# Performance work log

Measured on AMD Instinct MI355X. Metric: run time of the kernel, lower is better.

## Reference

```python
import jax, jax.numpy as jnp
import numpy as np

K = 3           # kernel_size
PAD = (K - 1) // 2
GC = 16         # group_channels (hardcoded in module)
EPS = 1e-5      # BatchNorm eps


def _extract_patches(x):
    # x: [B,C,H,W] -> [B,C,K*K,H,W], patch index = kh*K+kw (torch Unfold order)
    B, C, H, W = x.shape
    xp = jnp.pad(x, ((0, 0), (0, 0), (PAD, PAD), (PAD, PAD)))
    slices = [xp[:, :, i:i + H, j:j + W] for i in range(K) for j in range(K)]
    return jnp.stack(slices, axis=2)


def setup_inputs() -> dict:
    key = jax.random.key(0)
    ks = jax.random.split(key, 6)
    B, C, H, W = 4, 256, 128, 128
    Cr = C // 4                 # reduction_ratio = 4
    G = C // GC                 # groups = 16
    x = jax.random.normal(ks[0], (B, C, H, W), dtype=jnp.float32)
    # conv1: 1x1, C -> C/4, bias-free (followed by BN) + ReLU
    w1 = jax.random.normal(ks[1], (Cr, C), dtype=jnp.float32) * (1.0 / np.sqrt(C))
    bn_gamma = jnp.ones((Cr,), jnp.float32)
    bn_beta = jnp.zeros((Cr,), jnp.float32)
    bn_mean = jax.random.normal(ks[2], (Cr,), dtype=jnp.float32) * 0.1
    bn_var = jax.random.uniform(ks[3], (Cr,), dtype=jnp.float32, minval=0.5, maxval=1.5)
    # conv2: 1x1, C/4 -> K*K*groups, with bias, no norm/act
    w2 = jax.random.normal(ks[4], (K * K * G, Cr), dtype=jnp.float32) * (1.0 / np.sqrt(Cr))
    b2 = jax.random.normal(ks[5], (K * K * G,), dtype=jnp.float32) * 0.01
    return {"x": x, "w1": w1, "bn_gamma": bn_gamma, "bn_beta": bn_beta,
            "bn_mean": bn_mean, "bn_var": bn_var, "w2": w2, "b2": b2}


def reference(x, w1, bn_gamma, bn_beta, bn_mean, bn_var, w2, b2):
    B, C, H, W = x.shape
    G = C // GC
    # conv1 (1x1) + BN (inference) + ReLU
    h1 = jnp.einsum('bchw,oc->bohw', x, w1)
    inv_std = jax.lax.rsqrt(bn_var + EPS)
    h1 = (h1 - bn_mean[None, :, None, None]) * (bn_gamma * inv_std)[None, :, None, None] \
         + bn_beta[None, :, None, None]
    h1 = jax.nn.relu(h1)
    # conv2 (1x1) -> per-pixel dynamic kernels [B, G, K*K, H, W]
    wk = jnp.einsum('bchw,oc->bohw', h1, w2) + b2[None, :, None, None]
    wk = wk.reshape(B, G, K * K, H, W)
    # unfold x -> [B, G, GC, K*K, H, W], multiply by kernels and reduce over K*K
    patches = _extract_patches(x).reshape(B, G, GC, K * K, H, W)
    out = jnp.einsum('bgkhw,bgckhw->bgchw', wk, patches)
    return out.reshape(B, C, H, W)
```

## Files before the change

### kernel.cpp

```cpp
#include <hip/hip_runtime.h>

#define B_   4
#define C_   256
#define CR_  64
#define H_   128
#define W_   128
#define HW_  (H_ * W_)
#define G_   16
#define GC_  16
#define KO_  144
#define EPS_ 1e-5f

typedef __bf16 bf16x8 __attribute__((ext_vector_type(8)));
typedef __bf16 bf16x4 __attribute__((ext_vector_type(4)));
typedef float  f32x4  __attribute__((ext_vector_type(4)));

#define SX2 132
#define WKS 132

__global__ void prep_kernel(const float* __restrict__ w1,
                            const float* __restrict__ gamma,
                            const float* __restrict__ beta,
                            const float* __restrict__ mean,
                            const float* __restrict__ var,
                            const float* __restrict__ w2,
                            __bf16* __restrict__ w1frag,
                            __bf16* __restrict__ w2frag,
                            float* __restrict__ bias2) {
    int idx = blockIdx.x * 256 + threadIdx.x;
    if (idx < 16384) {
        int kc = idx >> 11, r = idx & 2047;
        int mt = r >> 9, l = (r >> 3) & 63, j = r & 7;
        int o = mt * 16 + (l & 15);
        int c = kc * 32 + 8 * (l >> 4) + j;
        float alpha = gamma[o] * rsqrtf(var[o] + EPS_);
        w1frag[idx] = (__bf16)(w1[o * C_ + c] * alpha);
        if (idx < CR_) {
            float a2 = gamma[idx] * rsqrtf(var[idx] + EPS_);
            bias2[idx] = beta[idx] - mean[idx] * a2;
        }
    } else if (idx < 16384 + 9216) {
        int i2 = idx - 16384;
        int mt = i2 >> 10, r = i2 & 1023;
        int kc2 = r >> 9, l = (r >> 3) & 63, j = r & 7;
        int o2 = mt * 16 + (l & 15);
        int cc = kc2 * 32 + 8 * (l >> 4) + j;
        w2frag[i2] = (__bf16)(w2[o2 * CR_ + cc]);
    }
}

__global__ __launch_bounds__(512, 4) void fused_kernel(
        const float* __restrict__ x,
        const __bf16* __restrict__ w1frag,
        const float* __restrict__ bias2,
        const __bf16* __restrict__ w2frag,
        const float* __restrict__ b2,
        float* __restrict__ out) {
    __shared__ __align__(16) char smem[71808];
    __bf16* xs    = (__bf16*)smem;
    __bf16* hbuf  = (__bf16*)(smem + 16896);
    __bf16* wkbuf = (__bf16*)(smem + 33792);
    __bf16* cbuf  = (__bf16*)smem;

    const int tid  = threadIdx.x;
    const int lane = tid & 63;
    const int wave = tid >> 6;
    const int wm = wave >> 2, wn = wave & 3;
    const int g = lane >> 4, n = lane & 15;

    const int bid = (blockIdx.x & 7) * 64 + (blockIdx.x >> 3);
    const int b   = bid >> 7;
    const int h   = bid & 127;

    const float* xrow = x + (size_t)b * C_ * HW_ + h * W_;

#pragma unroll
    for (int i = 0; i < 2; ++i) {
        int s = tid + 512 * i;
        int cl = s >> 5, f4i = s & 31;
        float4 v = *(const float4*)&xrow[(size_t)cl * HW_ + f4i * 4];
        *(bf16x4*)&xs[cl * SX2 + f4i * 4] =
            bf16x4{(__bf16)v.x, (__bf16)v.y, (__bf16)v.z, (__bf16)v.w};
    }
    __syncthreads();

    f32x4 acc1[2][2];
#pragma unroll
    for (int m = 0; m < 2; ++m)
#pragma unroll
        for (int t = 0; t < 2; ++t) acc1[m][t] = f32x4{0.f, 0.f, 0.f, 0.f};

    for (int kc = 0; kc < 8; ++kc) {
        const int buf = kc & 1;
        float4 nf[2];
        if (kc < 7) {
#pragma unroll
            for (int i = 0; i < 2; ++i) {
                int s = tid + 512 * i;
                int cl = s >> 5, f4i = s & 31;
                nf[i] = *(const float4*)&xrow[(size_t)(32 * (kc + 1) + cl) * HW_ + f4i * 4];
            }
        }
        bf16x8 a0 = *(const bf16x8*)&w1frag[((kc * 4 + 2 * wm + 0) * 64 + lane) * 8];
        bf16x8 a1 = *(const bf16x8*)&w1frag[((kc * 4 + 2 * wm + 1) * 64 + lane) * 8];
        const int base = buf * (32 * SX2);
        bf16x8 bt[2];
#pragma unroll
        for (int t = 0; t < 2; ++t)
#pragma unroll
            for (int j = 0; j < 8; ++j)
                bt[t][j] = xs[base + (8 * g + j) * SX2 + (2 * wn + t) * 16 + n];
#pragma unroll
        for (int t = 0; t < 2; ++t) {
            acc1[0][t] = __builtin_amdgcn_mfma_f32_16x16x32_bf16(a0, bt[t], acc1[0][t], 0, 0, 0);
            acc1[1][t] = __builtin_amdgcn_mfma_f32_16x16x32_bf16(a1, bt[t], acc1[1][t], 0, 0, 0);
        }
        if (kc < 7) {
            const int nb = (buf ^ 1) * (32 * SX2);
#pragma unroll
            for (int i = 0; i < 2; ++i) {
                int s = tid + 512 * i;
                int cl = s >> 5, f4i = s & 31;
                *(bf16x4*)&xs[nb + cl * SX2 + f4i * 4] =
                    bf16x4{(__bf16)nf[i].x, (__bf16)nf[i].y, (__bf16)nf[i].z, (__bf16)nf[i].w};
            }
        }
        __syncthreads();
    }

#pragma unroll
    for (int m = 0; m < 2; ++m) {
        const int Mo = (2 * wm + m) * 16 + 4 * g;
        float4 bv = *(const float4*)&bias2[Mo];
        float bj[4] = {bv.x, bv.y, bv.z, bv.w};
#pragma unroll
        for (int t = 0; t < 2; ++t) {
            const int px = (2 * wn + t) * 16 + n;
#pragma unroll
            for (int j = 0; j < 4; ++j)
                hbuf[(Mo + j) * SX2 + px] = (__bf16)fmaxf(acc1[m][t][j] + bj[j], 0.f);
        }
    }
    __syncthreads();

    f32x4 acc2[9];
#pragma unroll
    for (int m = 0; m < 9; ++m) acc2[m] = f32x4{0.f, 0.f, 0.f, 0.f};

#pragma unroll
    for (int kc2 = 0; kc2 < 2; ++kc2) {
        bf16x8 hb;
#pragma unroll
        for (int j = 0; j < 8; ++j)
            hb[j] = hbuf[(kc2 * 32 + 8 * g + j) * SX2 + wave * 16 + n];
#pragma unroll
        for (int mt = 0; mt < 9; ++mt) {
            bf16x8 a = *(const bf16x8*)&w2frag[((mt * 2 + kc2) * 64 + lane) * 8];
            acc2[mt] = __builtin_amdgcn_mfma_f32_16x16x32_bf16(a, hb, acc2[mt], 0, 0, 0);
        }
    }

#pragma unroll
    for (int mt = 0; mt < 9; ++mt) {
        const int o0 = mt * 16 + 4 * g;
        float4 bv = *(const float4*)&b2[o0];
        float bj[4] = {bv.x, bv.y, bv.z, bv.w};
#pragma unroll
        for (int j = 0; j < 4; ++j)
            wkbuf[(o0 + j) * WKS + wave * 16 + n] = (__bf16)(acc2[mt][j] + bj[j]);
    }
    __syncthreads();

    const int q  = tid & 31;
    const int cp = tid >> 5;
    const int w0 = q * 4;
    const bool ql = (q == 0), qr = (q == 31);

    float4 pf[6];
#pragma unroll
    for (int i = 0; i < 6; ++i) {
        int s = tid + 512 * i;
        int rr = s >> 5, f4i = s & 31;
        int cl = rr / 3, r = rr - 3 * cl;
        int gh = h - 1 + r;
        pf[i] = float4{0.f, 0.f, 0.f, 0.f};
        if (gh >= 0 && gh < H_)
            pf[i] = *(const float4*)&x[((size_t)(b * C_ + cl)) * HW_ + gh * W_ + f4i * 4];
    }
#pragma unroll
    for (int i = 0; i < 6; ++i) {
        int s = tid + 512 * i;
        int rr = s >> 5, f4i = s & 31;
        *(bf16x4*)&cbuf[rr * SX2 + f4i * 4] =
            bf16x4{(__bf16)pf[i].x, (__bf16)pf[i].y, (__bf16)pf[i].z, (__bf16)pf[i].w};
    }
    __syncthreads();

    for (int chunk = 0; chunk < 8; ++chunk) {
        const int ch0 = chunk * 32;
        if (chunk < 7) {
#pragma unroll
            for (int i = 0; i < 6; ++i) {
                int s = tid + 512 * i;
                int rr = s >> 5, f4i = s & 31;
                int cl = rr / 3, r = rr - 3 * cl;
                int gh = h - 1 + r;
                pf[i] = float4{0.f, 0.f, 0.f, 0.f};
                if (gh >= 0 && gh < H_)
                    pf[i] = *(const float4*)&x[((size_t)(b * C_ + ch0 + 32 + cl)) * HW_ + gh * W_ + f4i * 4];
            }
        }

        const int gq = chunk * 2 + (cp >> 3);
        float4 wk4[9];
#pragma unroll
        for (int k = 0; k < 9; ++k) {
            bf16x4 v = *(const bf16x4*)&wkbuf[(gq * 9 + k) * WKS + w0];
            wk4[k] = float4{(float)v[0], (float)v[1], (float)v[2], (float)v[3]};
        }

#pragma unroll
        for (int i2 = 0; i2 < 2; ++i2) {
            const int cl = cp * 2 + i2;
            const __bf16* bse = &cbuf[(cl * 3) * SX2 + w0];
            float4 acc = {0.f, 0.f, 0.f, 0.f};
#pragma unroll
            for (int dr = 0; dr < 3; ++dr) {
                bf16x4 cv = *(const bf16x4*)(bse + dr * SX2);
                float4 c = {(float)cv[0], (float)cv[1], (float)cv[2], (float)cv[3]};
                float lms = __shfl(c.w, lane - 1);
                float rms = __shfl(c.x, lane + 1);
                float lm = ql ? 0.f : lms;
                float rm = qr ? 0.f : rms;
                float4 t0 = wk4[3 * dr + 0];
                float4 t1 = wk4[3 * dr + 1];
                float4 t2 = wk4[3 * dr + 2];
                acc.x = fmaf(t0.x, lm,  acc.x);
                acc.y = fmaf(t0.y, c.x, acc.y);
                acc.z = fmaf(t0.z, c.y, acc.z);
                acc.w = fmaf(t0.w, c.z, acc.w);
                acc.x = fmaf(t1.x, c.x, acc.x);
                acc.y = fmaf(t1.y, c.y, acc.y);
                acc.z = fmaf(t1.z, c.z, acc.z);
                acc.w = fmaf(t1.w, c.w, acc.w);
                acc.x = fmaf(t2.x, c.y, acc.x);
                acc.y = fmaf(t2.y, c.z, acc.y);
                acc.z = fmaf(t2.z, c.w, acc.z);
                acc.w = fmaf(t2.w, rm,  acc.w);
            }
            f32x4 av = {acc.x, acc.y, acc.z, acc.w};
            __builtin_nontemporal_store(av,
                (f32x4*)&out[((size_t)(b * C_ + ch0 + cl)) * HW_ + h * W_ + w0]);
        }
        __syncthreads();
        if (chunk < 7) {
#pragma unroll
            for (int i = 0; i < 6; ++i) {
                int s = tid + 512 * i;
                int rr = s >> 5, f4i = s & 31;
                *(bf16x4*)&cbuf[rr * SX2 + f4i * 4] =
                    bf16x4{(__bf16)pf[i].x, (__bf16)pf[i].y, (__bf16)pf[i].z, (__bf16)pf[i].w};
            }
        }
        __syncthreads();
    }
}

extern "C" void kernel_launch(void* const* d_in, const int* in_sizes, int n_in,
                              void* d_out, int out_size, void* d_ws, size_t ws_size,
                              hipStream_t stream) {
    const float* x     = (const float*)d_in[0];
    const float* w1    = (const float*)d_in[1];
    const float* gamma = (const float*)d_in[2];
    const float* beta  = (const float*)d_in[3];
    const float* mean  = (const float*)d_in[4];
    const float* var   = (const float*)d_in[5];
    const float* w2    = (const float*)d_in[6];
    const float* b2    = (const float*)d_in[7];
    float* out = (float*)d_out;

    char* ws = (char*)d_ws;
    __bf16* w1frag = (__bf16*)(ws);
    __bf16* w2frag = (__bf16*)(ws + (32 << 10));
    float*  bias2  = (float*)(ws + (56 << 10));

    hipLaunchKernelGGL(prep_kernel, dim3(100), dim3(256), 0, stream,
                       w1, gamma, beta, mean, var, w2, w1frag, w2frag, bias2);
    hipLaunchKernelGGL(fused_kernel, dim3(512), dim3(512), 0, stream,
                       x, w1frag, bias2, w2frag, b2, out);
}
```

Baseline: 52.72 us.

## Load conv taps directly from global into registers, drop LDS staging and barriers

The dynamic-conv phase no longer stages three input rows per channel through shared memory in bf16 chunks with block-wide barriers. Each wave now owns two groups and streams its channels' three rows straight from global memory into double-buffered registers, with fp32 precision kept. Shared memory shrinks because wkbuf now aliases the x staging area, which could raise occupancy. The cost is more register pressure and less coalesced, wave-local prefetching that relies on cache hits for the neighbouring rows.

```diff
diff --git a/kernel.cpp b/kernel.cpp
--- a/kernel.cpp
+++ b/kernel.cpp
@@ -56,11 +56,10 @@
         const __bf16* __restrict__ w2frag,
         const float* __restrict__ b2,
         float* __restrict__ out) {
-    __shared__ __align__(16) char smem[71808];
+    __shared__ __align__(16) char smem[54912];
+    __bf16* wkbuf = (__bf16*)smem;
     __bf16* xs    = (__bf16*)smem;
-    __bf16* hbuf  = (__bf16*)(smem + 16896);
-    __bf16* wkbuf = (__bf16*)(smem + 33792);
-    __bf16* cbuf  = (__bf16*)smem;
+    __bf16* hbuf  = (__bf16*)(smem + 38016);
 
     const int tid  = threadIdx.x;
     const int lane = tid & 63;
@@ -171,63 +170,43 @@
     }
     __syncthreads();
 
-    const int q  = tid & 31;
-    const int cp = tid >> 5;
-    const int w0 = q * 4;
+    const int q   = lane & 31;
+    const int sub = lane >> 5;
+    const int w0  = q * 4;
     const bool ql = (q == 0), qr = (q == 31);
-
-    float4 pf[6];
-#pragma unroll
-    for (int i = 0; i < 6; ++i) {
-        int s = tid + 512 * i;
-        int rr = s >> 5, f4i = s & 31;
-        int cl = rr / 3, r = rr - 3 * cl;
-        int gh = h - 1 + r;
-        pf[i] = float4{0.f, 0.f, 0.f, 0.f};
-        if (gh >= 0 && gh < H_)
-            pf[i] = *(const float4*)&x[((size_t)(b * C_ + cl)) * HW_ + gh * W_ + f4i * 4];
-    }
-#pragma unroll
-    for (int i = 0; i < 6; ++i) {
-        int s = tid + 512 * i;
-        int rr = s >> 5, f4i = s & 31;
-        *(bf16x4*)&cbuf[rr * SX2 + f4i * 4] =
-            bf16x4{(__bf16)pf[i].x, (__bf16)pf[i].y, (__bf16)pf[i].z, (__bf16)pf[i].w};
-    }
-    __syncthreads();
-
-    for (int chunk = 0; chunk < 8; ++chunk) {
-        const int ch0 = chunk * 32;
-        if (chunk < 7) {
-#pragma unroll
-            for (int i = 0; i < 6; ++i) {
-                int s = tid + 512 * i;
-                int rr = s >> 5, f4i = s & 31;
-                int cl = rr / 3, r = rr - 3 * cl;
-                int gh = h - 1 + r;
-                pf[i] = float4{0.f, 0.f, 0.f, 0.f};
-                if (gh >= 0 && gh < H_)
-                    pf[i] = *(const float4*)&x[((size_t)(b * C_ + ch0 + 32 + cl)) * HW_ + gh * W_ + f4i * 4];
-            }
-        }
-
-        const int gq = chunk * 2 + (cp >> 3);
+    const bool h0ok = (h > 0), h2ok = (h < H_ - 1);
+
+    for (int half = 0; half < 2; ++half) {
+        const int gq = 2 * wave + half;
         float4 wk4[9];
 #pragma unroll
         for (int k = 0; k < 9; ++k) {
             bf16x4 v = *(const bf16x4*)&wkbuf[(gq * 9 + k) * WKS + w0];
             wk4[k] = float4{(float)v[0], (float)v[1], (float)v[2], (float)v[3]};
         }
-
-#pragma unroll
-        for (int i2 = 0; i2 < 2; ++i2) {
-            const int cl = cp * 2 + i2;
-            const __bf16* bse = &cbuf[(cl * 3) * SX2 + w0];
+        const int cbase = gq * GC_ + sub;
+
+        float4 bufA[3], bufB[3];
+        {
+            const float* xc = x + ((size_t)(b * C_ + cbase)) * HW_ + (h - 1) * W_ + w0;
+            bufA[0] = h0ok ? *(const float4*)xc : float4{0.f, 0.f, 0.f, 0.f};
+            bufA[1] = *(const float4*)(xc + W_);
+            bufA[2] = h2ok ? *(const float4*)(xc + 2 * W_) : float4{0.f, 0.f, 0.f, 0.f};
+        }
+#pragma unroll
+        for (int p = 0; p < 8; ++p) {
+            float4* cur = (p & 1) ? bufB : bufA;
+            float4* nxt = (p & 1) ? bufA : bufB;
+            if (p < 7) {
+                const float* xc = x + ((size_t)(b * C_ + cbase + 2 * (p + 1))) * HW_ + (h - 1) * W_ + w0;
+                nxt[0] = h0ok ? *(const float4*)xc : float4{0.f, 0.f, 0.f, 0.f};
+                nxt[1] = *(const float4*)(xc + W_);
+                nxt[2] = h2ok ? *(const float4*)(xc + 2 * W_) : float4{0.f, 0.f, 0.f, 0.f};
+            }
             float4 acc = {0.f, 0.f, 0.f, 0.f};
 #pragma unroll
             for (int dr = 0; dr < 3; ++dr) {
-                bf16x4 cv = *(const bf16x4*)(bse + dr * SX2);
-                float4 c = {(float)cv[0], (float)cv[1], (float)cv[2], (float)cv[3]};
+                float4 c = cur[dr];
                 float lms = __shfl(c.w, lane - 1);
                 float rms = __shfl(c.x, lane + 1);
                 float lm = ql ? 0.f : lms;
@@ -250,19 +229,8 @@
             }
             f32x4 av = {acc.x, acc.y, acc.z, acc.w};
             __builtin_nontemporal_store(av,
-                (f32x4*)&out[((size_t)(b * C_ + ch0 + cl)) * HW_ + h * W_ + w0]);
-        }
-        __syncthreads();
-        if (chunk < 7) {
-#pragma unroll
-            for (int i = 0; i < 6; ++i) {
-                int s = tid + 512 * i;
-                int rr = s >> 5, f4i = s & 31;
-                *(bf16x4*)&cbuf[rr * SX2 + f4i * 4] =
-                    bf16x4{(__bf16)pf[i].x, (__bf16)pf[i].y, (__bf16)pf[i].z, (__bf16)pf[i].w};
-            }
-        }
-        __syncthreads();
+                (f32x4*)&out[((size_t)(b * C_ + cbase + 2 * p)) * HW_ + h * W_ + w0]);
+        }
     }
 }
 
```

New measurement: 43.24 us. 1.22x faster.
